# Kernel tuning notes

Measured on AMD Instinct MI355X. Metric: run time of the kernel, lower is better.

Reference implementation:

```python
import jax, jax.numpy as jnp
import numpy as np

N_NODES = 20000
N_EDGES = 320000
N_GRAPHS = 512
VOCAB = 32
D = 256
K_HOPS = 4
EPS = 1e-5


def setup_inputs() -> dict:
    key = jax.random.key(0)
    ks = jax.random.split(key, 16)
    s = 0.02
    return {
        "x": jax.random.randint(ks[0], (N_NODES,), 0, VOCAB),
        "edge_index": jax.random.randint(ks[1], (2, N_EDGES), 0, N_NODES),
        "batch": jnp.sort(jax.random.randint(ks[2], (N_NODES,), 0, N_GRAPHS)),
        "node_table": jax.random.normal(ks[3], (VOCAB, D)) * s,
        "sg_W": jax.random.normal(ks[4], (D, D)) * s,
        "sg_b": jnp.zeros((D,)),
        "W1": jax.random.normal(ks[5], (D, 2 * D)) * s,
        "b1": jnp.zeros((2 * D,)),
        "g1": jnp.ones((2 * D,)),
        "be1": jnp.zeros((2 * D,)),
        "W2": jax.random.normal(ks[6], (2 * D, D)) * s,
        "b2": jnp.zeros((D,)),
        "g2": jnp.ones((D,)),
        "be2": jnp.zeros((D,)),
        "W3": jax.random.normal(ks[7], (D, 1)) * s,
        "b3": jnp.zeros((1,)),
    }


def _batchnorm(z, g, b):
    # BatchNorm1d in training-mode math (batch statistics), deterministic.
    m = z.mean(axis=0)
    v = z.var(axis=0)
    return (z - m) * jax.lax.rsqrt(v + EPS) * g + b


def reference(x, edge_index, batch, node_table, sg_W, sg_b,
              W1, b1, g1, be1, W2, b2, g2, be2, W3, b3):
    n = node_table.shape[0] and x.shape[0]  # N nodes
    h = node_table[x]  # [N, D] node embedding lookup (NodeEncoder)

    # SGConv: add self-loops, symmetric normalization, K hops, then Linear.
    loop = jnp.arange(n, dtype=edge_index.dtype)
    src = jnp.concatenate([edge_index[0], loop])
    dst = jnp.concatenate([edge_index[1], loop])
    deg = jax.ops.segment_sum(jnp.ones_like(dst, dtype=h.dtype), dst, num_segments=n)
    dinv = jnp.where(deg > 0, jax.lax.rsqrt(jnp.maximum(deg, 1.0)), 0.0)
    norm = (dinv[src] * dinv[dst])[:, None]  # [E+N, 1]
    for _ in range(K_HOPS):
        h = jax.ops.segment_sum(h[src] * norm, dst, num_segments=n)
    h = h @ sg_W + sg_b  # [N, D]

    # global_add_pool over graphs (dropout = identity in eval)
    hg = jax.ops.segment_sum(h, batch, num_segments=N_GRAPHS)  # [G, D]

    hg = jax.nn.relu(_batchnorm(hg @ W1 + b1, g1, be1))  # [G, 2D]
    hg = jax.nn.relu(_batchnorm(hg @ W2 + b2, g2, be2))  # [G, D]
    return hg @ W3 + b3  # [G, num_tasks]
```

## Files before the change

kernel.cpp:

```cpp
#include <hip/hip_runtime.h>

#define N_NODES  20000
#define N_EDGES  320000
#define N_GRAPHS 512
#define VOCAB    32
#define D        256
#define TWO_D    512
#define EPS      1e-5f
#define CAP      64
#define HB       (N_NODES / 16)


__device__ __forceinline__ unsigned int pack_bf2(float a, float b) {
    unsigned int ua = __float_as_uint(a);
    unsigned int ub = __float_as_uint(b);
    ua = (ua + 0x7FFFu + ((ua >> 16) & 1u)) >> 16;
    ub = (ub + 0x7FFFu + ((ub >> 16) & 1u)) >> 16;
    return ua | (ub << 16);
}
__device__ __forceinline__ float bf_lo(unsigned int v) { return __uint_as_float(v << 16); }
__device__ __forceinline__ float bf_hi(unsigned int v) { return __uint_as_float(v & 0xFFFF0000u); }


__global__ __launch_bounds__(512) void zero_fold_kernel(const int* __restrict__ batch,
                                                        int* __restrict__ cnt,
                                                        float* __restrict__ cs1,
                                                        float* __restrict__ cs2,
                                                        int* __restrict__ gstart,
                                                        const float* __restrict__ table,
                                                        const float* __restrict__ sgW,
                                                        const float* __restrict__ sg_b,
                                                        const float* __restrict__ W1,
                                                        float* __restrict__ G,
                                                        float* __restrict__ u) {
    __shared__ float trow[D];
    __shared__ float frow[D];
    int bid = blockIdx.x, tid = threadIdx.x;
    if (bid < 40) {
        int i = bid * 512 + tid;
        if (i < N_NODES) {
            cnt[i] = 0;
            int b = batch[i];
            if (i == 0) { for (int g = 0; g <= b; ++g) gstart[g] = 0; }
            else { int pb = batch[i - 1]; for (int g = pb + 1; g <= b; ++g) gstart[g] = i; }
            if (i == N_NODES - 1) { for (int g = b + 1; g <= N_GRAPHS; ++g) gstart[g] = N_NODES; }
        }
        if (i < 2 * TWO_D) cs1[i] = 0.f;
        if (i < 2 * D) cs2[i] = 0.f;
    } else {
        int r = bid - 40;
        if (r < VOCAB) {
            if (tid < D) trow[tid] = table[r * D + tid];
            __syncthreads();
            if (tid < D) {
                float acc = 0.f;
                for (int k = 0; k < D; ++k) acc += trow[k] * sgW[k * D + tid];
                frow[tid] = acc;
            }
        } else {
            if (tid < D) frow[tid] = sg_b[tid];
        }
        __syncthreads();
        float acc = 0.f;
        for (int k = 0; k < D; ++k) acc += frow[k] * W1[k * TWO_D + tid];
        float* dst = (r < VOCAB) ? (G + r * TWO_D) : u;
        dst[tid] = acc;
    }
}


__global__ __launch_bounds__(256) void bucket_kernel(const int* __restrict__ src,
                                                     const int* __restrict__ dst,
                                                     int* __restrict__ cnt,
                                                     int* __restrict__ buckets) {
    int e = blockIdx.x * 256 + threadIdx.x;
    if (e >= N_EDGES) return;
    int d = dst[e];
    int slot = atomicAdd(&cnt[d], 1);
    if (slot < CAP) buckets[d * CAP + slot] = src[e];
}


__global__ __launch_bounds__(256) void hop1_kernel(const int* __restrict__ x,
                                                   const int* __restrict__ cnt,
                                                   const int* __restrict__ buckets,
                                                   unsigned int* __restrict__ rout) {
    int node = (blockIdx.x << 4) | (threadIdx.x >> 4);
    int sub = threadIdx.x & 15;
    int f0 = sub * 2, f1 = f0 + 1;
    int cd = cnt[node];
    float dn = rsqrtf((float)(cd + 1));
    int xf = x[node];
    float ax = (xf == f0) ? dn : 0.f;
    float ay = (xf == f1) ? dn : 0.f;
    float bx = 0.f, by = 0.f;
    int n = min(cd, CAP);
    const int* bk = buckets + node * CAP;
    int j = 0;
    for (; j + 2 <= n; j += 2) {
        int s0 = bk[j], s1 = bk[j + 1];
        int xs0 = x[s0], xs1 = x[s1];
        float d0 = rsqrtf((float)(cnt[s0] + 1));
        float d1 = rsqrtf((float)(cnt[s1] + 1));
        ax += (xs0 == f0) ? d0 : 0.f;
        ay += (xs0 == f1) ? d0 : 0.f;
        bx += (xs1 == f0) ? d1 : 0.f;
        by += (xs1 == f1) ? d1 : 0.f;
    }
    if (j < n) {
        int s0 = bk[j];
        int xs0 = x[s0];
        float d0 = rsqrtf((float)(cnt[s0] + 1));
        ax += (xs0 == f0) ? d0 : 0.f;
        ay += (xs0 == f1) ? d0 : 0.f;
    }
    float q = 1.f / (float)(cd + 1);
    rout[node * 16 + sub] = pack_bf2(q * (ax + bx), q * (ay + by));
}


__global__ __launch_bounds__(256) void hop_kernel(const unsigned int* __restrict__ rin,
                                                  unsigned int* __restrict__ rout,
                                                  const int* __restrict__ cnt,
                                                  const int* __restrict__ buckets) {
    int node = (blockIdx.x << 4) | (threadIdx.x >> 4);
    int sub = threadIdx.x & 15;
    int cd = cnt[node];
    unsigned int self = rin[node * 16 + sub];
    float ax = bf_lo(self), ay = bf_hi(self);
    float bx = 0.f, by = 0.f, cx = 0.f, cy = 0.f, dx = 0.f, dy = 0.f;
    int n = min(cd, CAP);
    const int* bk = buckets + node * CAP;
    int j = 0;
    for (; j + 4 <= n; j += 4) {
        int s0 = bk[j], s1 = bk[j + 1], s2 = bk[j + 2], s3 = bk[j + 3];
        unsigned int v0 = rin[s0 * 16 + sub], v1 = rin[s1 * 16 + sub];
        unsigned int v2 = rin[s2 * 16 + sub], v3 = rin[s3 * 16 + sub];
        ax += bf_lo(v0); ay += bf_hi(v0);
        bx += bf_lo(v1); by += bf_hi(v1);
        cx += bf_lo(v2); cy += bf_hi(v2);
        dx += bf_lo(v3); dy += bf_hi(v3);
    }
    for (; j < n; ++j) {
        unsigned int v = rin[bk[j] * 16 + sub];
        ax += bf_lo(v); ay += bf_hi(v);
    }
    float q = 1.f / (float)(cd + 1);
    rout[node * 16 + sub] = pack_bf2(q * (ax + bx + cx + dx), q * (ay + by + cy + dy));
}


__global__ __launch_bounds__(256) void lin1p_kernel(const unsigned int* __restrict__ M,
                                                    const int* __restrict__ cnt,
                                                    const int* __restrict__ gstart,
                                                    const float* __restrict__ G,
                                                    const float* __restrict__ u,
                                                    const float* __restrict__ b1,
                                                    float* __restrict__ z1,
                                                    float* __restrict__ cs1) {
    __shared__ float S[8 * VOCAB];
    __shared__ float gcnt[8];
    int g0 = blockIdx.x * 8;
    int tid = threadIdx.x;
    int grp = tid >> 5, f = tid & 31;
    int g = g0 + grp;
    int lo = gstart[g], hi = gstart[g + 1];
    float s = 0.f;
    for (int i = lo; i < hi; ++i) {
        unsigned int v = M[i * 16 + (f >> 1)];
        float rv = sqrtf((float)(cnt[i] + 1));
        s += ((f & 1) ? bf_hi(v) : bf_lo(v)) * rv;
    }
    S[grp * 32 + f] = s;
    if (f == 0) gcnt[grp] = (float)(hi - lo);
    __syncthreads();
    float a0[8], a1[8];
#pragma unroll
    for (int i = 0; i < 8; ++i) { a0[i] = 0.f; a1[i] = 0.f; }
    for (int k = 0; k < VOCAB; ++k) {
        float w0 = G[k * TWO_D + tid];
        float w1 = G[k * TWO_D + tid + 256];
#pragma unroll
        for (int i = 0; i < 8; ++i) {
            float r = S[i * VOCAB + k];
            a0[i] += r * w0; a1[i] += r * w1;
        }
    }
    float u0 = u[tid], u1 = u[tid + 256];
    float c0 = b1[tid], c1 = b1[tid + 256];
    float s0 = 0.f, ss0 = 0.f, s1 = 0.f, ss1 = 0.f;
#pragma unroll
    for (int i = 0; i < 8; ++i) {
        float gc = gcnt[i];
        float z0v = a0[i] + gc * u0 + c0;
        float z1v = a1[i] + gc * u1 + c1;
        z1[(g0 + i) * TWO_D + tid]       = z0v;
        z1[(g0 + i) * TWO_D + tid + 256] = z1v;
        s0 += z0v; ss0 += z0v * z0v;
        s1 += z1v; ss1 += z1v * z1v;
    }
    atomicAdd(&cs1[tid], s0);
    atomicAdd(&cs1[TWO_D + tid], ss0);
    atomicAdd(&cs1[tid + 256], s1);
    atomicAdd(&cs1[TWO_D + tid + 256], ss1);
}


__global__ __launch_bounds__(256) void lin2_kernel(const float* __restrict__ z1,
                                                   const float* __restrict__ cs1,
                                                   const float* __restrict__ g1,
                                                   const float* __restrict__ be1,
                                                   const float* __restrict__ W2,
                                                   const float* __restrict__ b2,
                                                   float* __restrict__ z2,
                                                   float* __restrict__ cs2) {
    __shared__ float A[TWO_D], C[TWO_D];
    __shared__ float rows[4 * TWO_D];
    int tid = threadIdx.x;
    int g0 = blockIdx.x * 4;
    for (int k = tid; k < TWO_D; k += 256) {
        float m = cs1[k] * (1.f / N_GRAPHS);
        float var = cs1[TWO_D + k] * (1.f / N_GRAPHS) - m * m;
        float a = rsqrtf(var + EPS) * g1[k];
        A[k] = a;
        C[k] = be1[k] - m * a;
    }
    __syncthreads();
    for (int idx = tid; idx < 4 * TWO_D; idx += 256) {
        int k = idx & (TWO_D - 1);
        float v = z1[g0 * TWO_D + idx] * A[k] + C[k];
        rows[idx] = v > 0.f ? v : 0.f;
    }
    __syncthreads();
    float acc[4] = {0.f, 0.f, 0.f, 0.f};
    for (int k = 0; k < TWO_D; ++k) {
        float wv = W2[k * D + tid];
        acc[0] += rows[k] * wv;
        acc[1] += rows[TWO_D + k] * wv;
        acc[2] += rows[2 * TWO_D + k] * wv;
        acc[3] += rows[3 * TWO_D + k] * wv;
    }
    float bb = b2[tid];
    float s = 0.f, ss = 0.f;
#pragma unroll
    for (int i = 0; i < 4; ++i) {
        float zv = acc[i] + bb;
        z2[(g0 + i) * D + tid] = zv;
        s += zv; ss += zv * zv;
    }
    atomicAdd(&cs2[tid], s);
    atomicAdd(&cs2[D + tid], ss);
}


__global__ __launch_bounds__(64) void head_kernel(const float* __restrict__ z2,
                                                  const float* __restrict__ cs2,
                                                  const float* __restrict__ g2,
                                                  const float* __restrict__ be2,
                                                  const float* __restrict__ W3,
                                                  const float* __restrict__ b3,
                                                  float* __restrict__ out) {
    __shared__ float A[D], C[D];
    int g = blockIdx.x;
    int lane = threadIdx.x;
    for (int k = lane; k < D; k += 64) {
        float m = cs2[k] * (1.f / N_GRAPHS);
        float var = cs2[D + k] * (1.f / N_GRAPHS) - m * m;
        float a = rsqrtf(var + EPS) * g2[k];
        A[k] = a;
        C[k] = be2[k] - m * a;
    }
    __syncthreads();
    float acc = 0.f;
    for (int k = lane; k < D; k += 64) {
        float v = z2[g * D + k] * A[k] + C[k];
        v = v > 0.f ? v : 0.f;
        acc += v * W3[k];
    }
    for (int off = 32; off; off >>= 1) acc += __shfl_down(acc, off);
    if (lane == 0) out[g] = acc + b3[0];
}


extern "C" void kernel_launch(void* const* d_in, const int* in_sizes, int n_in,
                              void* d_out, int out_size, void* d_ws, size_t ws_size,
                              hipStream_t stream) {
    const int*   x     = (const int*)d_in[0];
    const int*   e_src = (const int*)d_in[1];
    const int*   e_dst = (const int*)d_in[1] + N_EDGES;
    const int*   batch = (const int*)d_in[2];
    const float* table = (const float*)d_in[3];
    const float* sg_W  = (const float*)d_in[4];
    const float* sg_b  = (const float*)d_in[5];
    const float* W1    = (const float*)d_in[6];
    const float* b1    = (const float*)d_in[7];
    const float* g1    = (const float*)d_in[8];
    const float* be1   = (const float*)d_in[9];
    const float* W2    = (const float*)d_in[10];
    const float* b2    = (const float*)d_in[11];
    const float* g2    = (const float*)d_in[12];
    const float* be2   = (const float*)d_in[13];
    const float* W3    = (const float*)d_in[14];
    const float* b3    = (const float*)d_in[15];
    float*       out   = (float*)d_out;

    char* p = (char*)d_ws;
    auto alloc = [&](size_t bytes) { char* q = p; p += (bytes + 15) & ~size_t(15); return q; };
    unsigned int* m_a = (unsigned int*)alloc((size_t)N_NODES * 16 * 4);
    unsigned int* m_b = (unsigned int*)alloc((size_t)N_NODES * 16 * 4);
    int*   cnt     = (int*)  alloc((size_t)N_NODES * 4);
    int*   buckets = (int*)  alloc((size_t)N_NODES * CAP * 4);
    int*   gstart  = (int*)  alloc((size_t)(N_GRAPHS + 1) * 4);
    float* G       = (float*)alloc((size_t)VOCAB * TWO_D * 4);
    float* u       = (float*)alloc((size_t)TWO_D * 4);
    float* z1      = (float*)alloc((size_t)N_GRAPHS * TWO_D * 4);
    float* z2      = (float*)alloc((size_t)N_GRAPHS * D * 4);
    float* cs1     = (float*)alloc((size_t)2 * TWO_D * 4);
    float* cs2     = (float*)alloc((size_t)2 * D * 4);

    zero_fold_kernel<<<73, 512, 0, stream>>>(batch, cnt, cs1, cs2, gstart,
                                             table, sg_W, sg_b, W1, G, u);
    bucket_kernel<<<(N_EDGES + 255) / 256, 256, 0, stream>>>(e_src, e_dst, cnt, buckets);

    hop1_kernel<<<HB, 256, 0, stream>>>(x, cnt, buckets, m_b);
    hop_kernel <<<HB, 256, 0, stream>>>(m_b, m_a, cnt, buckets);
    hop_kernel <<<HB, 256, 0, stream>>>(m_a, m_b, cnt, buckets);
    hop_kernel <<<HB, 256, 0, stream>>>(m_b, m_a, cnt, buckets);

    lin1p_kernel<<<N_GRAPHS / 8, 256, 0, stream>>>(m_a, cnt, gstart, G, u, b1, z1, cs1);
    lin2_kernel<<<N_GRAPHS / 4, 256, 0, stream>>>(z1, cs1, g1, be1, W2, b2, z2, cs2);
    head_kernel<<<N_GRAPHS, 64, 0, stream>>>(z2, cs2, g2, be2, W3, b3, out);
}
```

Baseline: 120.8 us.

## Fuse last hop with graph pooling and shuffle-broadcast bucket neighbor indices

```diff
diff --git a/kernel.cpp b/kernel.cpp
--- a/kernel.cpp
+++ b/kernel.cpp
@@ -26,6 +26,7 @@
                                                         int* __restrict__ cnt,
                                                         float* __restrict__ cs1,
                                                         float* __restrict__ cs2,
+                                                        float* __restrict__ S,
                                                         int* __restrict__ gstart,
                                                         const float* __restrict__ table,
                                                         const float* __restrict__ sgW,
@@ -47,6 +48,7 @@
         }
         if (i < 2 * TWO_D) cs1[i] = 0.f;
         if (i < 2 * D) cs2[i] = 0.f;
+        if (i < N_GRAPHS * VOCAB) S[i] = 0.f;
     } else {
         int r = bid - 40;
         if (r < VOCAB) {
@@ -87,6 +89,7 @@
                                                    unsigned int* __restrict__ rout) {
     int node = (blockIdx.x << 4) | (threadIdx.x >> 4);
     int sub = threadIdx.x & 15;
+    int qbase = (threadIdx.x & 63) & 48;
     int f0 = sub * 2, f1 = f0 + 1;
     int cd = cnt[node];
     float dn = rsqrtf((float)(cd + 1));
@@ -96,23 +99,28 @@
     float bx = 0.f, by = 0.f;
     int n = min(cd, CAP);
     const int* bk = buckets + node * CAP;
-    int j = 0;
-    for (; j + 2 <= n; j += 2) {
-        int s0 = bk[j], s1 = bk[j + 1];
-        int xs0 = x[s0], xs1 = x[s1];
-        float d0 = rsqrtf((float)(cnt[s0] + 1));
-        float d1 = rsqrtf((float)(cnt[s1] + 1));
-        ax += (xs0 == f0) ? d0 : 0.f;
-        ay += (xs0 == f1) ? d0 : 0.f;
-        bx += (xs1 == f0) ? d1 : 0.f;
-        by += (xs1 == f1) ? d1 : 0.f;
-    }
-    if (j < n) {
-        int s0 = bk[j];
-        int xs0 = x[s0];
-        float d0 = rsqrtf((float)(cnt[s0] + 1));
-        ax += (xs0 == f0) ? d0 : 0.f;
-        ay += (xs0 == f1) ? d0 : 0.f;
+    for (int w = 0; w < n; w += 16) {
+        int lw = min(16, n - w);
+        int bkv = bk[w + sub];
+        int j = 0;
+        for (; j + 2 <= lw; j += 2) {
+            int s0 = __shfl(bkv, qbase + j);
+            int s1 = __shfl(bkv, qbase + j + 1);
+            int x0 = x[s0], x1 = x[s1];
+            float d0 = rsqrtf((float)(cnt[s0] + 1));
+            float d1 = rsqrtf((float)(cnt[s1] + 1));
+            ax += (x0 == f0) ? d0 : 0.f;
+            ay += (x0 == f1) ? d0 : 0.f;
+            bx += (x1 == f0) ? d1 : 0.f;
+            by += (x1 == f1) ? d1 : 0.f;
+        }
+        if (j < lw) {
+            int s0 = __shfl(bkv, qbase + j);
+            int x0 = x[s0];
+            float d0 = rsqrtf((float)(cnt[s0] + 1));
+            ax += (x0 == f0) ? d0 : 0.f;
+            ay += (x0 == f1) ? d0 : 0.f;
+        }
     }
     float q = 1.f / (float)(cd + 1);
     rout[node * 16 + sub] = pack_bf2(q * (ax + bx), q * (ay + by));
@@ -125,54 +133,94 @@
                                                   const int* __restrict__ buckets) {
     int node = (blockIdx.x << 4) | (threadIdx.x >> 4);
     int sub = threadIdx.x & 15;
+    int qbase = (threadIdx.x & 63) & 48;
     int cd = cnt[node];
     unsigned int self = rin[node * 16 + sub];
     float ax = bf_lo(self), ay = bf_hi(self);
     float bx = 0.f, by = 0.f, cx = 0.f, cy = 0.f, dx = 0.f, dy = 0.f;
     int n = min(cd, CAP);
     const int* bk = buckets + node * CAP;
-    int j = 0;
-    for (; j + 4 <= n; j += 4) {
-        int s0 = bk[j], s1 = bk[j + 1], s2 = bk[j + 2], s3 = bk[j + 3];
-        unsigned int v0 = rin[s0 * 16 + sub], v1 = rin[s1 * 16 + sub];
-        unsigned int v2 = rin[s2 * 16 + sub], v3 = rin[s3 * 16 + sub];
-        ax += bf_lo(v0); ay += bf_hi(v0);
-        bx += bf_lo(v1); by += bf_hi(v1);
-        cx += bf_lo(v2); cy += bf_hi(v2);
-        dx += bf_lo(v3); dy += bf_hi(v3);
-    }
-    for (; j < n; ++j) {
-        unsigned int v = rin[bk[j] * 16 + sub];
-        ax += bf_lo(v); ay += bf_hi(v);
+    for (int w = 0; w < n; w += 16) {
+        int lw = min(16, n - w);
+        int bkv = bk[w + sub];
+        int j = 0;
+        for (; j + 4 <= lw; j += 4) {
+            int s0 = __shfl(bkv, qbase + j);
+            int s1 = __shfl(bkv, qbase + j + 1);
+            int s2 = __shfl(bkv, qbase + j + 2);
+            int s3 = __shfl(bkv, qbase + j + 3);
+            unsigned int v0 = rin[s0 * 16 + sub], v1 = rin[s1 * 16 + sub];
+            unsigned int v2 = rin[s2 * 16 + sub], v3 = rin[s3 * 16 + sub];
+            ax += bf_lo(v0); ay += bf_hi(v0);
+            bx += bf_lo(v1); by += bf_hi(v1);
+            cx += bf_lo(v2); cy += bf_hi(v2);
+            dx += bf_lo(v3); dy += bf_hi(v3);
+        }
+        for (; j < lw; ++j) {
+            int s = __shfl(bkv, qbase + j);
+            unsigned int v = rin[s * 16 + sub];
+            ax += bf_lo(v); ay += bf_hi(v);
+        }
     }
     float q = 1.f / (float)(cd + 1);
     rout[node * 16 + sub] = pack_bf2(q * (ax + bx + cx + dx), q * (ay + by + cy + dy));
 }
 
 
-__global__ __launch_bounds__(256) void lin1p_kernel(const unsigned int* __restrict__ M,
+__global__ __launch_bounds__(256) void hop4s_kernel(const unsigned int* __restrict__ rin,
                                                     const int* __restrict__ cnt,
-                                                    const int* __restrict__ gstart,
-                                                    const float* __restrict__ G,
-                                                    const float* __restrict__ u,
-                                                    const float* __restrict__ b1,
-                                                    float* __restrict__ z1,
-                                                    float* __restrict__ cs1) {
+                                                    const int* __restrict__ buckets,
+                                                    const int* __restrict__ batch,
+                                                    float* __restrict__ S) {
+    int node = (blockIdx.x << 4) | (threadIdx.x >> 4);
+    int sub = threadIdx.x & 15;
+    int qbase = (threadIdx.x & 63) & 48;
+    int cd = cnt[node];
+    unsigned int self = rin[node * 16 + sub];
+    float ax = bf_lo(self), ay = bf_hi(self);
+    float bx = 0.f, by = 0.f, cx = 0.f, cy = 0.f, dx = 0.f, dy = 0.f;
+    int n = min(cd, CAP);
+    const int* bk = buckets + node * CAP;
+    for (int w = 0; w < n; w += 16) {
+        int lw = min(16, n - w);
+        int bkv = bk[w + sub];
+        int j = 0;
+        for (; j + 4 <= lw; j += 4) {
+            int s0 = __shfl(bkv, qbase + j);
+            int s1 = __shfl(bkv, qbase + j + 1);
+            int s2 = __shfl(bkv, qbase + j + 2);
+            int s3 = __shfl(bkv, qbase + j + 3);
+            unsigned int v0 = rin[s0 * 16 + sub], v1 = rin[s1 * 16 + sub];
+            unsigned int v2 = rin[s2 * 16 + sub], v3 = rin[s3 * 16 + sub];
+            ax += bf_lo(v0); ay += bf_hi(v0);
+            bx += bf_lo(v1); by += bf_hi(v1);
+            cx += bf_lo(v2); cy += bf_hi(v2);
+            dx += bf_lo(v3); dy += bf_hi(v3);
+        }
+        for (; j < lw; ++j) {
+            int s = __shfl(bkv, qbase + j);
+            unsigned int v = rin[s * 16 + sub];
+            ax += bf_lo(v); ay += bf_hi(v);
+        }
+    }
+    float dinv = rsqrtf((float)(cd + 1));
+    int g = batch[node];
+    atomicAdd(&S[g * VOCAB + sub * 2],     dinv * (ax + bx + cx + dx));
+    atomicAdd(&S[g * VOCAB + sub * 2 + 1], dinv * (ay + by + cy + dy));
+}
+
+
+__global__ __launch_bounds__(256) void lin1_kernel(const float* __restrict__ S_,
+                                                   const int* __restrict__ gstart,
+                                                   const float* __restrict__ G,
+                                                   const float* __restrict__ u,
+                                                   const float* __restrict__ b1,
+                                                   float* __restrict__ z1,
+                                                   float* __restrict__ cs1) {
     __shared__ float S[8 * VOCAB];
-    __shared__ float gcnt[8];
     int g0 = blockIdx.x * 8;
     int tid = threadIdx.x;
-    int grp = tid >> 5, f = tid & 31;
-    int g = g0 + grp;
-    int lo = gstart[g], hi = gstart[g + 1];
-    float s = 0.f;
-    for (int i = lo; i < hi; ++i) {
-        unsigned int v = M[i * 16 + (f >> 1)];
-        float rv = sqrtf((float)(cnt[i] + 1));
-        s += ((f & 1) ? bf_hi(v) : bf_lo(v)) * rv;
-    }
-    S[grp * 32 + f] = s;
-    if (f == 0) gcnt[grp] = (float)(hi - lo);
+    S[tid] = S_[g0 * VOCAB + tid];
     __syncthreads();
     float a0[8], a1[8];
 #pragma unroll
@@ -191,7 +239,7 @@
     float s0 = 0.f, ss0 = 0.f, s1 = 0.f, ss1 = 0.f;
 #pragma unroll
     for (int i = 0; i < 8; ++i) {
-        float gc = gcnt[i];
+        float gc = (float)(gstart[g0 + i + 1] - gstart[g0 + i]);
         float z0v = a0[i] + gc * u0 + c0;
         float z1v = a1[i] + gc * u1 + c1;
         z1[(g0 + i) * TWO_D + tid]       = z0v;
@@ -311,6 +359,7 @@
     int*   cnt     = (int*)  alloc((size_t)N_NODES * 4);
     int*   buckets = (int*)  alloc((size_t)N_NODES * CAP * 4);
     int*   gstart  = (int*)  alloc((size_t)(N_GRAPHS + 1) * 4);
+    float* S       = (float*)alloc((size_t)N_GRAPHS * VOCAB * 4);
     float* G       = (float*)alloc((size_t)VOCAB * TWO_D * 4);
     float* u       = (float*)alloc((size_t)TWO_D * 4);
     float* z1      = (float*)alloc((size_t)N_GRAPHS * TWO_D * 4);
@@ -318,16 +367,16 @@
     float* cs1     = (float*)alloc((size_t)2 * TWO_D * 4);
     float* cs2     = (float*)alloc((size_t)2 * D * 4);
 
-    zero_fold_kernel<<<73, 512, 0, stream>>>(batch, cnt, cs1, cs2, gstart,
+    zero_fold_kernel<<<73, 512, 0, stream>>>(batch, cnt, cs1, cs2, S, gstart,
                                              table, sg_W, sg_b, W1, G, u);
     bucket_kernel<<<(N_EDGES + 255) / 256, 256, 0, stream>>>(e_src, e_dst, cnt, buckets);
 
-    hop1_kernel<<<HB, 256, 0, stream>>>(x, cnt, buckets, m_b);
-    hop_kernel <<<HB, 256, 0, stream>>>(m_b, m_a, cnt, buckets);
-    hop_kernel <<<HB, 256, 0, stream>>>(m_a, m_b, cnt, buckets);
-    hop_kernel <<<HB, 256, 0, stream>>>(m_b, m_a, cnt, buckets);
-
-    lin1p_kernel<<<N_GRAPHS / 8, 256, 0, stream>>>(m_a, cnt, gstart, G, u, b1, z1, cs1);
+    hop1_kernel <<<HB, 256, 0, stream>>>(x, cnt, buckets, m_b);
+    hop_kernel  <<<HB, 256, 0, stream>>>(m_b, m_a, cnt, buckets);
+    hop_kernel  <<<HB, 256, 0, stream>>>(m_a, m_b, cnt, buckets);
+    hop4s_kernel<<<HB, 256, 0, stream>>>(m_b, cnt, buckets, batch, S);
+
+    lin1_kernel<<<N_GRAPHS / 8, 256, 0, stream>>>(S, gstart, G, u, b1, z1, cs1);
     lin2_kernel<<<N_GRAPHS / 4, 256, 0, stream>>>(z1, cs1, g1, be1, W2, b2, z2, cs2);
     head_kernel<<<N_GRAPHS, 64, 0, stream>>>(z2, cs2, g2, be2, W3, b3, out);
 }
```

New measurement: 116.9 us. 1.03x faster.
